# Performance work log

Hardware: AMD Instinct MI355X
Metric: run time of the kernel (lower is better)

Reference implementation:

```python
import jax, jax.numpy as jnp
import numpy as np


def setup_inputs() -> dict:
    key = jax.random.key(0)
    ks = jax.random.split(key, 10)
    B, HD, CD = 8192, 1024, 1024
    stdv = 1.0 / np.sqrt(HD)
    inp = {
        "hprev": jax.random.normal(ks[0], (B, HD), dtype=jnp.float32),
        "cprev": jax.random.normal(ks[1], (B, CD), dtype=jnp.float32),
        "w_hi": jax.random.uniform(ks[2], (HD, CD), jnp.float32, -stdv, stdv),
        "b_hi": jax.random.uniform(ks[3], (1, CD), jnp.float32, -stdv, stdv),
        "w_hf": jax.random.uniform(ks[4], (HD, CD), jnp.float32, -stdv, stdv),
        "b_hf": jax.random.uniform(ks[5], (1, CD), jnp.float32, -stdv, stdv),
        "w_hg": jax.random.uniform(ks[6], (HD, CD), jnp.float32, -stdv, stdv),
        "b_hg": jax.random.uniform(ks[7], (1, CD), jnp.float32, -stdv, stdv),
        "w_ho": jax.random.uniform(ks[8], (HD, CD), jnp.float32, -stdv, stdv),
        "b_ho": jax.random.uniform(ks[9], (1, CD), jnp.float32, -stdv, stdv),
    }
    return inp


def reference(hprev, cprev, w_hi, b_hi, w_hf, b_hf, w_hg, b_hg, w_ho, b_ho):
    # LSTM cell gates driven only by previous hidden state.
    i = jax.nn.sigmoid(hprev @ w_hi + b_hi)   # input gate  [B, CD]
    f = jax.nn.sigmoid(hprev @ w_hf + b_hf)   # forget gate [B, CD]
    g = jnp.tanh(hprev @ w_hg + b_hg)         # cell candidate
    o = jax.nn.sigmoid(hprev @ w_ho + b_ho)   # output gate
    cprime = f * cprev + i * g
    hprime = o * jnp.tanh(cprime)
    return (hprime, cprime)
```

## Files before the change

kernel.cpp:

```cpp
#include <hip/hip_runtime.h>
#include <hip/hip_bf16.h>
#include <stdint.h>

typedef short short8 __attribute__((ext_vector_type(8)));
typedef float f32x4 __attribute__((ext_vector_type(4)));
typedef unsigned short ushort4v __attribute__((ext_vector_type(4)));

#define MDIM 8192
#define KDIM 1024
#define NDIM 1024

#define BM 128
#define BN 64
#define BK 64
#define NKSTEP (KDIM / BK)


__device__ __forceinline__ unsigned short f2bf(float f) {
  union { float f; unsigned int u; } v; v.f = f;
  unsigned int u = v.u;
  u += 0x7fffu + ((u >> 16) & 1u);
  return (unsigned short)(u >> 16);
}

__device__ __forceinline__ void load_lds16(const void* gsrc, void* ldst) {
  __builtin_amdgcn_global_load_lds(
      (__attribute__((address_space(1))) void*)gsrc,
      (__attribute__((address_space(3))) void*)ldst,
      16, 0, 0);
}

__device__ __forceinline__ float fast_sigmoid(float x) {
  return 1.0f / (1.0f + __expf(-x));
}

__device__ __forceinline__ float fast_tanh(float x) {
  x = fminf(30.0f, fmaxf(-30.0f, x));
  float e = __expf(-2.0f * x);
  return (1.0f - e) / (1.0f + e);
}


__global__ void convert_h_kernel(const float* __restrict__ in,
                                 unsigned short* __restrict__ out, int n4) {
  int idx = blockIdx.x * blockDim.x + threadIdx.x;
  int stride = gridDim.x * blockDim.x;
  for (int i = idx; i < n4; i += stride) {
    float4 v = reinterpret_cast<const float4*>(in)[i];
    ushort4v o;
    o.x = f2bf(v.x); o.y = f2bf(v.y); o.z = f2bf(v.z); o.w = f2bf(v.w);
    reinterpret_cast<ushort4v*>(out)[i] = o;
  }
}

__global__ void convert_w_kernel(const float* __restrict__ w0,
                                 const float* __restrict__ w1,
                                 const float* __restrict__ w2,
                                 const float* __restrict__ w3,
                                 unsigned short* __restrict__ wT) {
  __shared__ float tile[64][65];
  int g = blockIdx.z;
  const float* w = (g == 0) ? w0 : (g == 1) ? w1 : (g == 2) ? w2 : w3;
  int k0 = blockIdx.y * 64;
  int n0 = blockIdx.x * 64;
  int tx = threadIdx.x;
  int ty = threadIdx.y;
#pragma unroll
  for (int j = 0; j < 16; ++j) {
    int kk = ty * 16 + j;
    tile[kk][tx] = w[(size_t)(k0 + kk) * NDIM + n0 + tx];
  }
  __syncthreads();
  unsigned short* dst = wT + (size_t)g * NDIM * KDIM;
#pragma unroll
  for (int j = 0; j < 16; ++j) {
    int nn = ty * 16 + j;
    dst[(size_t)(n0 + nn) * KDIM + k0 + tx] = f2bf(tile[tx][nn]);
  }
}


__global__ __launch_bounds__(256, 2) void lstm_fused_gemm(
    const unsigned short* __restrict__ hbf,
    const unsigned short* __restrict__ wT,
    const float* __restrict__ cprev,
    const float* __restrict__ b_i, const float* __restrict__ b_f,
    const float* __restrict__ b_g, const float* __restrict__ b_o,
    float* __restrict__ out)
{
  __shared__ unsigned char lds[48 * 1024];
  const int tid = threadIdx.x;
  const int lane = tid & 63;
  const int wave = tid >> 6;

  int bid = blockIdx.x;
  int swz = (bid & 7) * 128 + (bid >> 3);
  int mb = swz >> 4;
  int nb = swz & 15;
  int brow = mb * BM;
  int bcol = nb * BN;

  const int wr = wave >> 1, wc = wave & 1;
  const int wrow = wr * 64, wcol = wc * 32;

  uint32_t offA[4], offB[8];
#pragma unroll
  for (int j = 0; j < 4; ++j) {
    int c = j * 256 + tid;
    int row = c >> 3, slot = c & 7;
    offA[j] = (uint32_t)((brow + row) * (KDIM * 2) + ((slot ^ (row & 7)) * 16));
  }
#pragma unroll
  for (int j = 0; j < 8; ++j) {
    int c = j * 256 + tid;
    int g = c >> 9;
    int row = (c >> 3) & 63;
    int slot = c & 7;
    offB[j] = (uint32_t)((g * NDIM + bcol + row) * (KDIM * 2) +
                         ((slot ^ (row & 7)) * 16));
  }

  const int h = lane >> 4;
  const int r15 = lane & 15;
  const int s = lane & 7;

  f32x4 acc[4][4][2];
#pragma unroll
  for (int g = 0; g < 4; ++g)
#pragma unroll
    for (int mf = 0; mf < 4; ++mf)
#pragma unroll
      for (int nf = 0; nf < 2; ++nf)
        acc[g][mf][nf] = (f32x4){0.f, 0.f, 0.f, 0.f};

  const char* hbase = (const char*)hbf;
  const char* wbase = (const char*)wT;

  for (int t = 0; t < NKSTEP; ++t) {
    const char* ha = hbase + t * 128;
    const char* wa = wbase + t * 128;
#pragma unroll
    for (int j = 0; j < 4; ++j)
      load_lds16(ha + offA[j], lds + tid * 16 + j * 4096);
#pragma unroll
    for (int j = 0; j < 8; ++j)
      load_lds16(wa + offB[j], lds + 16384 + tid * 16 + j * 4096);
    __syncthreads();

#pragma unroll
    for (int kk = 0; kk < 2; ++kk) {
      short8 a[4];
#pragma unroll
      for (int mf = 0; mf < 4; ++mf) {
        int off = (wrow + mf * 16 + r15) * 128 + (((kk * 4 + h) ^ s) * 16);
        a[mf] = *reinterpret_cast<const short8*>(lds + off);
      }
#pragma unroll
      for (int g = 0; g < 4; ++g) {
#pragma unroll
        for (int nf = 0; nf < 2; ++nf) {
          int off = 16384 + g * 8192 +
                    (wcol + nf * 16 + r15) * 128 + (((kk * 4 + h) ^ s) * 16);
          short8 b = *reinterpret_cast<const short8*>(lds + off);
#pragma unroll
          for (int mf = 0; mf < 4; ++mf)
            acc[g][mf][nf] = __builtin_amdgcn_mfma_f32_16x16x32_bf16(
                a[mf], b, acc[g][mf][nf], 0, 0, 0);
        }
      }
    }
    __syncthreads();
  }

  const size_t outCstride = (size_t)MDIM * NDIM;
#pragma unroll
  for (int nf = 0; nf < 2; ++nf) {
    int cc = bcol + wcol + nf * 16 + r15;
    float bi = b_i[cc];
    float bff = b_f[cc];
    float bg = b_g[cc];
    float bo = b_o[cc];
#pragma unroll
    for (int mf = 0; mf < 4; ++mf) {
#pragma unroll
      for (int j = 0; j < 4; ++j) {
        int rr = brow + wrow + mf * 16 + h * 4 + j;
        size_t base = (size_t)rr * NDIM + cc;
        float pi = acc[0][mf][nf][j] + bi;
        float pf = acc[1][mf][nf][j] + bff;
        float pg = acc[2][mf][nf][j] + bg;
        float po = acc[3][mf][nf][j] + bo;
        float iv = fast_sigmoid(pi);
        float fv = fast_sigmoid(pf);
        float gv = fast_tanh(pg);
        float ov = fast_sigmoid(po);
        float cp = fv * cprev[base] + iv * gv;
        float hp = ov * fast_tanh(cp);
        out[base] = hp;
        out[outCstride + base] = cp;
      }
    }
  }
}


extern "C" void kernel_launch(void* const* d_in, const int* in_sizes, int n_in,
                              void* d_out, int out_size, void* d_ws, size_t ws_size,
                              hipStream_t stream) {
  const float* hprev = (const float*)d_in[0];
  const float* cprev = (const float*)d_in[1];
  const float* w_hi  = (const float*)d_in[2];
  const float* b_hi  = (const float*)d_in[3];
  const float* w_hf  = (const float*)d_in[4];
  const float* b_hf  = (const float*)d_in[5];
  const float* w_hg  = (const float*)d_in[6];
  const float* b_hg  = (const float*)d_in[7];
  const float* w_ho  = (const float*)d_in[8];
  const float* b_ho  = (const float*)d_in[9];
  float* out = (float*)d_out;

  unsigned short* hbf = (unsigned short*)d_ws;
  unsigned short* wT  = (unsigned short*)((char*)d_ws + (size_t)MDIM * KDIM * 2);

  convert_h_kernel<<<2048, 256, 0, stream>>>(hprev, hbf, MDIM * KDIM / 4);
  convert_w_kernel<<<dim3(16, 16, 4), dim3(64, 4, 1), 0, stream>>>(
      w_hi, w_hf, w_hg, w_ho, wT);
  lstm_fused_gemm<<<1024, 256, 0, stream>>>(hbf, wT, cprev,
                                            b_hi, b_hf, b_hg, b_ho, out);
}
```

Baseline: 96.46 us.

## Restructure fused LSTM GEMM into double-buffered 256x64 tiles with interleaved staging

Replaces the single-buffered 128x64 block GEMM with 512-thread blocks computing 256-row tiles. It uses a 128KB double-buffered LDS ring and splits each K-step into halves, so global-to-LDS loads for the next tile are issued between MFMA clusters. Explicit barriers, waitcnt and setprio control the overlap. The aim is to hide global load latency and raise reuse of the weight tiles, at the cost of dropping the LDS XOR swizzle (possible bank conflicts) and limiting occupancy to one large block per CU because of the LDS footprint.

New measurement: 103.1 us. 6.9% more time.

```diff
diff --git a/kernel.cpp b/kernel.cpp
--- a/kernel.cpp
+++ b/kernel.cpp
@@ -9,11 +9,7 @@
 #define MDIM 8192
 #define KDIM 1024
 #define NDIM 1024
-
-#define BM 128
-#define BN 64
-#define BK 64
-#define NKSTEP (KDIM / BK)
+#define NKT  16
 
 
 __device__ __forceinline__ unsigned short f2bf(float f) {
@@ -80,7 +76,31 @@
 }
 
 
-__global__ __launch_bounds__(256, 2) void lstm_fused_gemm(
+#define LDS_BUF   65536
+#define LDS_KH    16384
+#define LDS_B_OFF 32768
+
+#define STAGE_A(kh, h, nb_, tn) \
+  load_lds16(hb + aoff + (h) * 262144 + (tn) * 128 + (kh) * 64, \
+             lds + (nb_) + (kh) * LDS_KH + (h) * 8192 + tid * 16)
+#define STAGE_B(kh, h, nb_, tn) \
+  load_lds16(wb + ((h) ? boff1 : boff0) + (tn) * 128 + (kh) * 64, \
+             lds + (nb_) + LDS_B_OFF + (kh) * LDS_KH + (h) * 8192 + tid * 16)
+
+#define RD_A(cb_, kk, m) \
+  (*(const short8*)(lds + (cb_) + (kk) * LDS_KH + \
+                    (wr * 128 + (m) * 16 + r15) * 64 + hh * 16))
+#define RD_B(cb_, kk, g) \
+  (*(const short8*)(lds + (cb_) + LDS_B_OFF + (kk) * LDS_KH + \
+                    ((g) * 64 + wc * 16 + r15) * 64 + hh * 16))
+
+#define BARRIER() __builtin_amdgcn_s_barrier()
+#define WAIT_LGKM0() do { \
+    asm volatile("s_waitcnt lgkmcnt(0)" ::: "memory"); \
+    __builtin_amdgcn_sched_barrier(0); } while (0)
+#define WAIT_VM4() asm volatile("s_waitcnt vmcnt(4)" ::: "memory")
+
+__global__ __launch_bounds__(512, 2) void lstm_fused_gemm(
     const unsigned short* __restrict__ hbf,
     const unsigned short* __restrict__ wT,
     const float* __restrict__ cprev,
@@ -88,117 +108,179 @@
     const float* __restrict__ b_g, const float* __restrict__ b_o,
     float* __restrict__ out)
 {
-  __shared__ unsigned char lds[48 * 1024];
-  const int tid = threadIdx.x;
+  extern __shared__ unsigned char lds[];
+  const int tid  = threadIdx.x;
   const int lane = tid & 63;
   const int wave = tid >> 6;
+  const int wr = wave >> 2;
+  const int wc = wave & 3;
+  const int r15 = lane & 15;
+  const int hh  = lane >> 4;
 
   int bid = blockIdx.x;
-  int swz = (bid & 7) * 128 + (bid >> 3);
-  int mb = swz >> 4;
-  int nb = swz & 15;
-  int brow = mb * BM;
-  int bcol = nb * BN;
-
-  const int wr = wave >> 1, wc = wave & 1;
-  const int wrow = wr * 64, wcol = wc * 32;
-
-  uint32_t offA[4], offB[8];
-#pragma unroll
-  for (int j = 0; j < 4; ++j) {
-    int c = j * 256 + tid;
-    int row = c >> 3, slot = c & 7;
-    offA[j] = (uint32_t)((brow + row) * (KDIM * 2) + ((slot ^ (row & 7)) * 16));
-  }
-#pragma unroll
-  for (int j = 0; j < 8; ++j) {
-    int c = j * 256 + tid;
-    int g = c >> 9;
-    int row = (c >> 3) & 63;
-    int slot = c & 7;
-    offB[j] = (uint32_t)((g * NDIM + bcol + row) * (KDIM * 2) +
-                         ((slot ^ (row & 7)) * 16));
-  }
-
-  const int h = lane >> 4;
-  const int r15 = lane & 15;
-  const int s = lane & 7;
-
-  f32x4 acc[4][4][2];
+  int loc = bid >> 3;
+  int mb = (bid & 7) * 4 + (loc >> 4);
+  int nb = loc & 15;
+  int brow = mb * 256;
+  int bcol = nb * 64;
+
+  const char* hb = (const char*)hbf;
+  const char* wb = (const char*)wT;
+  const int q  = tid & 3;
+  const int sr = tid >> 2;
+  const uint32_t aoff  = (uint32_t)((brow + sr) * 2048 + q * 16);
+  const uint32_t boff0 = (uint32_t)((((sr >> 6)) * 1024 + bcol + (sr & 63)) * 2048 + q * 16);
+  const uint32_t boff1 = (uint32_t)(((2 + (sr >> 6)) * 1024 + bcol + (sr & 63)) * 2048 + q * 16);
+
+  f32x4 acc[4][8];
 #pragma unroll
   for (int g = 0; g < 4; ++g)
 #pragma unroll
-    for (int mf = 0; mf < 4; ++mf)
-#pragma unroll
-      for (int nf = 0; nf < 2; ++nf)
-        acc[g][mf][nf] = (f32x4){0.f, 0.f, 0.f, 0.f};
-
-  const char* hbase = (const char*)hbf;
-  const char* wbase = (const char*)wT;
-
-  for (int t = 0; t < NKSTEP; ++t) {
-    const char* ha = hbase + t * 128;
-    const char* wa = wbase + t * 128;
-#pragma unroll
-    for (int j = 0; j < 4; ++j)
-      load_lds16(ha + offA[j], lds + tid * 16 + j * 4096);
-#pragma unroll
-    for (int j = 0; j < 8; ++j)
-      load_lds16(wa + offB[j], lds + 16384 + tid * 16 + j * 4096);
-    __syncthreads();
-
-#pragma unroll
-    for (int kk = 0; kk < 2; ++kk) {
-      short8 a[4];
-#pragma unroll
-      for (int mf = 0; mf < 4; ++mf) {
-        int off = (wrow + mf * 16 + r15) * 128 + (((kk * 4 + h) ^ s) * 16);
-        a[mf] = *reinterpret_cast<const short8*>(lds + off);
-      }
-#pragma unroll
-      for (int g = 0; g < 4; ++g) {
-#pragma unroll
-        for (int nf = 0; nf < 2; ++nf) {
-          int off = 16384 + g * 8192 +
-                    (wcol + nf * 16 + r15) * 128 + (((kk * 4 + h) ^ s) * 16);
-          short8 b = *reinterpret_cast<const short8*>(lds + off);
-#pragma unroll
-          for (int mf = 0; mf < 4; ++mf)
-            acc[g][mf][nf] = __builtin_amdgcn_mfma_f32_16x16x32_bf16(
-                a[mf], b, acc[g][mf][nf], 0, 0, 0);
-        }
-      }
-    }
-    __syncthreads();
-  }
-
-  const size_t outCstride = (size_t)MDIM * NDIM;
-#pragma unroll
-  for (int nf = 0; nf < 2; ++nf) {
-    int cc = bcol + wcol + nf * 16 + r15;
-    float bi = b_i[cc];
-    float bff = b_f[cc];
-    float bg = b_g[cc];
-    float bo = b_o[cc];
-#pragma unroll
-    for (int mf = 0; mf < 4; ++mf) {
-#pragma unroll
-      for (int j = 0; j < 4; ++j) {
-        int rr = brow + wrow + mf * 16 + h * 4 + j;
-        size_t base = (size_t)rr * NDIM + cc;
-        float pi = acc[0][mf][nf][j] + bi;
-        float pf = acc[1][mf][nf][j] + bff;
-        float pg = acc[2][mf][nf][j] + bg;
-        float po = acc[3][mf][nf][j] + bo;
-        float iv = fast_sigmoid(pi);
-        float fv = fast_sigmoid(pf);
-        float gv = fast_tanh(pg);
-        float ov = fast_sigmoid(po);
-        float cp = fv * cprev[base] + iv * gv;
-        float hp = ov * fast_tanh(cp);
-        out[base] = hp;
-        out[outCstride + base] = cp;
-      }
+    for (int m = 0; m < 8; ++m)
+      acc[g][m] = (f32x4){0.f, 0.f, 0.f, 0.f};
+
+  uint32_t cb = 0, nbuf = LDS_BUF;
+
+  STAGE_A(0, 0, cb, 0); STAGE_A(0, 1, cb, 0);
+  STAGE_B(0, 0, cb, 0); STAGE_B(0, 1, cb, 0);
+  STAGE_A(1, 0, cb, 0); STAGE_A(1, 1, cb, 0);
+  STAGE_B(1, 0, cb, 0); STAGE_B(1, 1, cb, 0);
+  WAIT_VM4();
+  BARRIER();
+
+  for (int t = 0; t < NKT; ++t) {
+    const int tn = (t + 1) & (NKT - 1);
+
+    short8 B0 = RD_B(cb, 0, 0), B1 = RD_B(cb, 0, 1),
+           B2 = RD_B(cb, 0, 2), B3 = RD_B(cb, 0, 3);
+    short8 A0 = RD_A(cb, 0, 0), A1 = RD_A(cb, 0, 1),
+           A2 = RD_A(cb, 0, 2), A3 = RD_A(cb, 0, 3);
+    STAGE_A(0, 0, nbuf, tn); STAGE_A(0, 1, nbuf, tn);
+    BARRIER();
+    WAIT_LGKM0();
+    __builtin_amdgcn_s_setprio(1);
+    acc[0][0] = __builtin_amdgcn_mfma_f32_16x16x32_bf16(A0, B0, acc[0][0], 0, 0, 0);
+    acc[1][0] = __builtin_amdgcn_mfma_f32_16x16x32_bf16(A0, B1, acc[1][0], 0, 0, 0);
+    acc[2][0] = __builtin_amdgcn_mfma_f32_16x16x32_bf16(A0, B2, acc[2][0], 0, 0, 0);
+    acc[3][0] = __builtin_amdgcn_mfma_f32_16x16x32_bf16(A0, B3, acc[3][0], 0, 0, 0);
+    acc[0][1] = __builtin_amdgcn_mfma_f32_16x16x32_bf16(A1, B0, acc[0][1], 0, 0, 0);
+    acc[1][1] = __builtin_amdgcn_mfma_f32_16x16x32_bf16(A1, B1, acc[1][1], 0, 0, 0);
+    acc[2][1] = __builtin_amdgcn_mfma_f32_16x16x32_bf16(A1, B2, acc[2][1], 0, 0, 0);
+    acc[3][1] = __builtin_amdgcn_mfma_f32_16x16x32_bf16(A1, B3, acc[3][1], 0, 0, 0);
+    acc[0][2] = __builtin_amdgcn_mfma_f32_16x16x32_bf16(A2, B0, acc[0][2], 0, 0, 0);
+    acc[1][2] = __builtin_amdgcn_mfma_f32_16x16x32_bf16(A2, B1, acc[1][2], 0, 0, 0);
+    acc[2][2] = __builtin_amdgcn_mfma_f32_16x16x32_bf16(A2, B2, acc[2][2], 0, 0, 0);
+    acc[3][2] = __builtin_amdgcn_mfma_f32_16x16x32_bf16(A2, B3, acc[3][2], 0, 0, 0);
+    acc[0][3] = __builtin_amdgcn_mfma_f32_16x16x32_bf16(A3, B0, acc[0][3], 0, 0, 0);
+    acc[1][3] = __builtin_amdgcn_mfma_f32_16x16x32_bf16(A3, B1, acc[1][3], 0, 0, 0);
+    acc[2][3] = __builtin_amdgcn_mfma_f32_16x16x32_bf16(A3, B2, acc[2][3], 0, 0, 0);
+    acc[3][3] = __builtin_amdgcn_mfma_f32_16x16x32_bf16(A3, B3, acc[3][3], 0, 0, 0);
+    __builtin_amdgcn_s_setprio(0);
+    BARRIER();
+
+    short8 A4 = RD_A(cb, 0, 4), A5 = RD_A(cb, 0, 5),
+           A6 = RD_A(cb, 0, 6), A7 = RD_A(cb, 0, 7);
+    STAGE_B(0, 0, nbuf, tn); STAGE_B(0, 1, nbuf, tn);
+    BARRIER();
+    WAIT_LGKM0();
+    __builtin_amdgcn_s_setprio(1);
+    acc[0][4] = __builtin_amdgcn_mfma_f32_16x16x32_bf16(A4, B0, acc[0][4], 0, 0, 0);
+    acc[1][4] = __builtin_amdgcn_mfma_f32_16x16x32_bf16(A4, B1, acc[1][4], 0, 0, 0);
+    acc[2][4] = __builtin_amdgcn_mfma_f32_16x16x32_bf16(A4, B2, acc[2][4], 0, 0, 0);
+    acc[3][4] = __builtin_amdgcn_mfma_f32_16x16x32_bf16(A4, B3, acc[3][4], 0, 0, 0);
+    acc[0][5] = __builtin_amdgcn_mfma_f32_16x16x32_bf16(A5, B0, acc[0][5], 0, 0, 0);
+    acc[1][5] = __builtin_amdgcn_mfma_f32_16x16x32_bf16(A5, B1, acc[1][5], 0, 0, 0);
+    acc[2][5] = __builtin_amdgcn_mfma_f32_16x16x32_bf16(A5, B2, acc[2][5], 0, 0, 0);
+    acc[3][5] = __builtin_amdgcn_mfma_f32_16x16x32_bf16(A5, B3, acc[3][5], 0, 0, 0);
+    acc[0][6] = __builtin_amdgcn_mfma_f32_16x16x32_bf16(A6, B0, acc[0][6], 0, 0, 0);
+    acc[1][6] = __builtin_amdgcn_mfma_f32_16x16x32_bf16(A6, B1, acc[1][6], 0, 0, 0);
+    acc[2][6] = __builtin_amdgcn_mfma_f32_16x16x32_bf16(A6, B2, acc[2][6], 0, 0, 0);
+    acc[3][6] = __builtin_amdgcn_mfma_f32_16x16x32_bf16(A6, B3, acc[3][6], 0, 0, 0);
+    acc[0][7] = __builtin_amdgcn_mfma_f32_16x16x32_bf16(A7, B0, acc[0][7], 0, 0, 0);
+    acc[1][7] = __builtin_amdgcn_mfma_f32_16x16x32_bf16(A7, B1, acc[1][7], 0, 0, 0);
+    acc[2][7] = __builtin_amdgcn_mfma_f32_16x16x32_bf16(A7, B2, acc[2][7], 0, 0, 0);
+    acc[3][7] = __builtin_amdgcn_mfma_f32_16x16x32_bf16(A7, B3, acc[3][7], 0, 0, 0);
+    __builtin_amdgcn_s_setprio(0);
+    WAIT_VM4();
+    BARRIER();
+
+    B0 = RD_B(cb, 1, 0); B1 = RD_B(cb, 1, 1);
+    B2 = RD_B(cb, 1, 2); B3 = RD_B(cb, 1, 3);
+    A0 = RD_A(cb, 1, 0); A1 = RD_A(cb, 1, 1);
+    A2 = RD_A(cb, 1, 2); A3 = RD_A(cb, 1, 3);
+    STAGE_A(1, 0, nbuf, tn); STAGE_A(1, 1, nbuf, tn);
+    BARRIER();
+    WAIT_LGKM0();
+    __builtin_amdgcn_s_setprio(1);
+    acc[0][0] = __builtin_amdgcn_mfma_f32_16x16x32_bf16(A0, B0, acc[0][0], 0, 0, 0);
+    acc[1][0] = __builtin_amdgcn_mfma_f32_16x16x32_bf16(A0, B1, acc[1][0], 0, 0, 0);
+    acc[2][0] = __builtin_amdgcn_mfma_f32_16x16x32_bf16(A0, B2, acc[2][0], 0, 0, 0);
+    acc[3][0] = __builtin_amdgcn_mfma_f32_16x16x32_bf16(A0, B3, acc[3][0], 0, 0, 0);
+    acc[0][1] = __builtin_amdgcn_mfma_f32_16x16x32_bf16(A1, B0, acc[0][1], 0, 0, 0);
+    acc[1][1] = __builtin_amdgcn_mfma_f32_16x16x32_bf16(A1, B1, acc[1][1], 0, 0, 0);
+    acc[2][1] = __builtin_amdgcn_mfma_f32_16x16x32_bf16(A1, B2, acc[2][1], 0, 0, 0);
+    acc[3][1] = __builtin_amdgcn_mfma_f32_16x16x32_bf16(A1, B3, acc[3][1], 0, 0, 0);
+    acc[0][2] = __builtin_amdgcn_mfma_f32_16x16x32_bf16(A2, B0, acc[0][2], 0, 0, 0);
+    acc[1][2] = __builtin_amdgcn_mfma_f32_16x16x32_bf16(A2, B1, acc[1][2], 0, 0, 0);
+    acc[2][2] = __builtin_amdgcn_mfma_f32_16x16x32_bf16(A2, B2, acc[2][2], 0, 0, 0);
+    acc[3][2] = __builtin_amdgcn_mfma_f32_16x16x32_bf16(A2, B3, acc[3][2], 0, 0, 0);
+    acc[0][3] = __builtin_amdgcn_mfma_f32_16x16x32_bf16(A3, B0, acc[0][3], 0, 0, 0);
+    acc[1][3] = __builtin_amdgcn_mfma_f32_16x16x32_bf16(A3, B1, acc[1][3], 0, 0, 0);
+    acc[2][3] = __builtin_amdgcn_mfma_f32_16x16x32_bf16(A3, B2, acc[2][3], 0, 0, 0);
+    acc[3][3] = __builtin_amdgcn_mfma_f32_16x16x32_bf16(A3, B3, acc[3][3], 0, 0, 0);
+    __builtin_amdgcn_s_setprio(0);
+    BARRIER();
+
+    A4 = RD_A(cb, 1, 4); A5 = RD_A(cb, 1, 5);
+    A6 = RD_A(cb, 1, 6); A7 = RD_A(cb, 1, 7);
+    STAGE_B(1, 0, nbuf, tn); STAGE_B(1, 1, nbuf, tn);
+    BARRIER();
+    WAIT_LGKM0();
+    __builtin_amdgcn_s_setprio(1);
+    acc[0][4] = __builtin_amdgcn_mfma_f32_16x16x32_bf16(A4, B0, acc[0][4], 0, 0, 0);
+    acc[1][4] = __builtin_amdgcn_mfma_f32_16x16x32_bf16(A4, B1, acc[1][4], 0, 0, 0);
+    acc[2][4] = __builtin_amdgcn_mfma_f32_16x16x32_bf16(A4, B2, acc[2][4], 0, 0, 0);
+    acc[3][4] = __builtin_amdgcn_mfma_f32_16x16x32_bf16(A4, B3, acc[3][4], 0, 0, 0);
+    acc[0][5] = __builtin_amdgcn_mfma_f32_16x16x32_bf16(A5, B0, acc[0][5], 0, 0, 0);
+    acc[1][5] = __builtin_amdgcn_mfma_f32_16x16x32_bf16(A5, B1, acc[1][5], 0, 0, 0);
+    acc[2][5] = __builtin_amdgcn_mfma_f32_16x16x32_bf16(A5, B2, acc[2][5], 0, 0, 0);
+    acc[3][5] = __builtin_amdgcn_mfma_f32_16x16x32_bf16(A5, B3, acc[3][5], 0, 0, 0);
+    acc[0][6] = __builtin_amdgcn_mfma_f32_16x16x32_bf16(A6, B0, acc[0][6], 0, 0, 0);
+    acc[1][6] = __builtin_amdgcn_mfma_f32_16x16x32_bf16(A6, B1, acc[1][6], 0, 0, 0);
+    acc[2][6] = __builtin_amdgcn_mfma_f32_16x16x32_bf16(A6, B2, acc[2][6], 0, 0, 0);
+    acc[3][6] = __builtin_amdgcn_mfma_f32_16x16x32_bf16(A6, B3, acc[3][6], 0, 0, 0);
+    acc[0][7] = __builtin_amdgcn_mfma_f32_16x16x32_bf16(A7, B0, acc[0][7], 0, 0, 0);
+    acc[1][7] = __builtin_amdgcn_mfma_f32_16x16x32_bf16(A7, B1, acc[1][7], 0, 0, 0);
+    acc[2][7] = __builtin_amdgcn_mfma_f32_16x16x32_bf16(A7, B2, acc[2][7], 0, 0, 0);
+    acc[3][7] = __builtin_amdgcn_mfma_f32_16x16x32_bf16(A7, B3, acc[3][7], 0, 0, 0);
+    __builtin_amdgcn_s_setprio(0);
+    WAIT_VM4();
+    BARRIER();
+
+    uint32_t tmp = cb; cb = nbuf; nbuf = tmp;
+  }
+
+  const size_t outC = (size_t)MDIM * NDIM;
+  const int cc = bcol + wc * 16 + r15;
+  const float bi = b_i[cc], bff = b_f[cc], bg = b_g[cc], bo = b_o[cc];
+#pragma unroll
+  for (int m = 0; m < 8; ++m) {
+#pragma unroll
+    for (int j = 0; j < 4; ++j) {
+      int rr = brow + wr * 128 + m * 16 + hh * 4 + j;
+      size_t base = (size_t)rr * NDIM + cc;
+      float pi = acc[0][m][j] + bi;
+      float pf = acc[1][m][j] + bff;
+      float pg = acc[2][m][j] + bg;
+      float po = acc[3][m][j] + bo;
+      float iv = fast_sigmoid(pi);
+      float fv = fast_sigmoid(pf);
+      float gv = fast_tanh(pg);
+      float ov = fast_sigmoid(po);
+      float cp = fv * cprev[base] + iv * gv;
+      float hp = ov * fast_tanh(cp);
+      out[base] = hp;
+      out[outC + base] = cp;
     }
   }
 }
@@ -225,6 +307,6 @@
   convert_h_kernel<<<2048, 256, 0, stream>>>(hprev, hbf, MDIM * KDIM / 4);
   convert_w_kernel<<<dim3(16, 16, 4), dim3(64, 4, 1), 0, stream>>>(
       w_hi, w_hf, w_hg, w_ho, wT);
-  lstm_fused_gemm<<<1024, 256, 0, stream>>>(hbf, wT, cprev,
-                                            b_hi, b_hf, b_hg, b_ho, out);
-}
+  lstm_fused_gemm<<<512, 512, 131072, stream>>>(hbf, wT, cprev,
+                                                b_hi, b_hf, b_hg, b_ho, out);
+}
```

## Rewrite fused LSTM GEMM with 4-stage LDS ring buffer and 512-thread tiles

Applied to the files above, without the earlier changes.

Replaces the single-buffered, sync-per-step GEMM with a 256x64 (per gate) tile computed by 8 waves. It uses a 4-slot LDS ring buffer (128KB dynamic shared memory), prefetching three K-chunks ahead with global_load_lds and interleaving staging with MFMA using explicit s_barrier, waitcnt and setprio. The aim is to hide global-load latency and raise data reuse per block, with a new swizzled LDS layout. The cost is large LDS use, which limits occupancy to about one block per CU, plus fragile hand-written wait counts and barriers.

Measured after the change: 101.2 us. 4.9% more time.

```diff
diff --git a/kernel.cpp b/kernel.cpp
--- a/kernel.cpp
+++ b/kernel.cpp
@@ -9,11 +9,7 @@
 #define MDIM 8192
 #define KDIM 1024
 #define NDIM 1024
-
-#define BM 128
-#define BN 64
-#define BK 64
-#define NKSTEP (KDIM / BK)
+#define NHALF 32
 
 
 __device__ __forceinline__ unsigned short f2bf(float f) {
@@ -80,7 +76,65 @@
 }
 
 
-__global__ __launch_bounds__(256, 2) void lstm_fused_gemm(
+#define SLOT_SZ 32768
+#define S0 0
+#define S1 32768
+#define S2 65536
+#define S3 98304
+
+#define BARRIER() __builtin_amdgcn_s_barrier()
+#define WAIT_LGKM0() do { \
+    asm volatile("s_waitcnt lgkmcnt(0)" ::: "memory"); \
+    __builtin_amdgcn_sched_barrier(0); } while (0)
+#define WAIT_VM8() asm volatile("s_waitcnt vmcnt(8)" ::: "memory")
+
+#define STAGE_A_H(koff, T) do { \
+    load_lds16(hb + srcA0 + (koff), lds + (T) + tid * 16); \
+    load_lds16(hb + srcA1 + (koff), lds + (T) + 8192 + tid * 16); } while (0)
+#define STAGE_B_H(koff, T) do { \
+    load_lds16(wb + srcB0 + (koff), lds + (T) + 16384 + tid * 16); \
+    load_lds16(wb + srcB1 + (koff), lds + (T) + 16384 + 8192 + tid * 16); } while (0)
+
+#define MFMA16(mb_) do { \
+  _Pragma("unroll") \
+  for (int mi = 0; mi < 4; ++mi) { \
+    _Pragma("unroll") \
+    for (int g = 0; g < 4; ++g) \
+      acc[g][(mb_) + mi] = __builtin_amdgcn_mfma_f32_16x16x32_bf16( \
+          Af[mi], Bf[g], acc[g][(mb_) + mi], 0, 0, 0); \
+  } } while (0)
+
+#define HALF(hidx, S, T) do { \
+    const uint32_t ko = (uint32_t)(((hidx) + 3) & (NHALF - 1)) * 64; \
+     \
+    short8 Bf[4], Af[4]; \
+    _Pragma("unroll") \
+    for (int g = 0; g < 4; ++g) \
+      Bf[g] = *(const short8*)(lds + (S) + 16384 + g * 4096 + b_off); \
+    _Pragma("unroll") \
+    for (int mi = 0; mi < 4; ++mi) \
+      Af[mi] = *(const short8*)(lds + (S) + a_off + mi * 1024); \
+    STAGE_A_H(ko, T); \
+    BARRIER(); \
+    WAIT_LGKM0(); \
+    __builtin_amdgcn_s_setprio(1); \
+    MFMA16(0); \
+    __builtin_amdgcn_s_setprio(0); \
+    BARRIER(); \
+     \
+    _Pragma("unroll") \
+    for (int mi = 0; mi < 4; ++mi) \
+      Af[mi] = *(const short8*)(lds + (S) + a_off + (4 + mi) * 1024); \
+    STAGE_B_H(ko, T); \
+    BARRIER(); \
+    WAIT_LGKM0(); \
+    __builtin_amdgcn_s_setprio(1); \
+    MFMA16(4); \
+    __builtin_amdgcn_s_setprio(0); \
+    WAIT_VM8(); \
+    BARRIER(); } while (0)
+
+__global__ __launch_bounds__(512, 2) void lstm_fused_gemm(
     const unsigned short* __restrict__ hbf,
     const unsigned short* __restrict__ wT,
     const float* __restrict__ cprev,
@@ -88,117 +142,81 @@
     const float* __restrict__ b_g, const float* __restrict__ b_o,
     float* __restrict__ out)
 {
-  __shared__ unsigned char lds[48 * 1024];
-  const int tid = threadIdx.x;
+  extern __shared__ unsigned char lds[];
+  const int tid  = threadIdx.x;
   const int lane = tid & 63;
   const int wave = tid >> 6;
+  const int wr = wave >> 2;
+  const int wc = wave & 3;
+  const int r15 = lane & 15;
+  const int hh  = lane >> 4;
 
   int bid = blockIdx.x;
-  int swz = (bid & 7) * 128 + (bid >> 3);
-  int mb = swz >> 4;
-  int nb = swz & 15;
-  int brow = mb * BM;
-  int bcol = nb * BN;
-
-  const int wr = wave >> 1, wc = wave & 1;
-  const int wrow = wr * 64, wcol = wc * 32;
-
-  uint32_t offA[4], offB[8];
-#pragma unroll
-  for (int j = 0; j < 4; ++j) {
-    int c = j * 256 + tid;
-    int row = c >> 3, slot = c & 7;
-    offA[j] = (uint32_t)((brow + row) * (KDIM * 2) + ((slot ^ (row & 7)) * 16));
-  }
-#pragma unroll
-  for (int j = 0; j < 8; ++j) {
-    int c = j * 256 + tid;
-    int g = c >> 9;
-    int row = (c >> 3) & 63;
-    int slot = c & 7;
-    offB[j] = (uint32_t)((g * NDIM + bcol + row) * (KDIM * 2) +
-                         ((slot ^ (row & 7)) * 16));
-  }
-
-  const int h = lane >> 4;
-  const int r15 = lane & 15;
-  const int s = lane & 7;
-
-  f32x4 acc[4][4][2];
+  int loc = bid >> 3;
+  int mb = (bid & 7) * 4 + (loc >> 4);
+  int nb = loc & 15;
+  int brow = mb * 256;
+  int bcol = nb * 64;
+
+  const char* hb = (const char*)hbf;
+  const char* wb = (const char*)wT;
+
+  const int sD = tid & 7;
+  const int pB = tid >> 3;
+  const int u  = sD ^ (pB & 7);
+  const int c16 = (u & 3) * 16;
+  const int rA0 = 2 * pB + (u >> 2);
+  const int rA1 = 128 + rA0;
+  const uint32_t srcA0 = (uint32_t)(brow + rA0) * 2048 + c16;
+  const uint32_t srcA1 = (uint32_t)(brow + rA1) * 2048 + c16;
+  const uint32_t srcB0 = (uint32_t)((rA0 >> 6) * 1024 + bcol + (rA0 & 63)) * 2048 + c16;
+  const uint32_t srcB1 = (uint32_t)((rA1 >> 6) * 1024 + bcol + (rA1 & 63)) * 2048 + c16;
+
+  const int slot16 = (((((r15 & 1) << 2) | hh) ^ (r15 >> 1)) * 16);
+  const uint32_t a_off = (uint32_t)(wr * 64 + (r15 >> 1)) * 128 + slot16;
+  const uint32_t b_off = (uint32_t)(wc * 8 + (r15 >> 1)) * 128 + slot16;
+
+  f32x4 acc[4][8];
 #pragma unroll
   for (int g = 0; g < 4; ++g)
 #pragma unroll
-    for (int mf = 0; mf < 4; ++mf)
-#pragma unroll
-      for (int nf = 0; nf < 2; ++nf)
-        acc[g][mf][nf] = (f32x4){0.f, 0.f, 0.f, 0.f};
-
-  const char* hbase = (const char*)hbf;
-  const char* wbase = (const char*)wT;
-
-  for (int t = 0; t < NKSTEP; ++t) {
-    const char* ha = hbase + t * 128;
-    const char* wa = wbase + t * 128;
-#pragma unroll
-    for (int j = 0; j < 4; ++j)
-      load_lds16(ha + offA[j], lds + tid * 16 + j * 4096);
-#pragma unroll
-    for (int j = 0; j < 8; ++j)
-      load_lds16(wa + offB[j], lds + 16384 + tid * 16 + j * 4096);
-    __syncthreads();
-
-#pragma unroll
-    for (int kk = 0; kk < 2; ++kk) {
-      short8 a[4];
-#pragma unroll
-      for (int mf = 0; mf < 4; ++mf) {
-        int off = (wrow + mf * 16 + r15) * 128 + (((kk * 4 + h) ^ s) * 16);
-        a[mf] = *reinterpret_cast<const short8*>(lds + off);
-      }
-#pragma unroll
-      for (int g = 0; g < 4; ++g) {
-#pragma unroll
-        for (int nf = 0; nf < 2; ++nf) {
-          int off = 16384 + g * 8192 +
-                    (wcol + nf * 16 + r15) * 128 + (((kk * 4 + h) ^ s) * 16);
-          short8 b = *reinterpret_cast<const short8*>(lds + off);
-#pragma unroll
-          for (int mf = 0; mf < 4; ++mf)
-            acc[g][mf][nf] = __builtin_amdgcn_mfma_f32_16x16x32_bf16(
-                a[mf], b, acc[g][mf][nf], 0, 0, 0);
-        }
-      }
-    }
-    __syncthreads();
-  }
-
-  const size_t outCstride = (size_t)MDIM * NDIM;
-#pragma unroll
-  for (int nf = 0; nf < 2; ++nf) {
-    int cc = bcol + wcol + nf * 16 + r15;
-    float bi = b_i[cc];
-    float bff = b_f[cc];
-    float bg = b_g[cc];
-    float bo = b_o[cc];
-#pragma unroll
-    for (int mf = 0; mf < 4; ++mf) {
-#pragma unroll
-      for (int j = 0; j < 4; ++j) {
-        int rr = brow + wrow + mf * 16 + h * 4 + j;
-        size_t base = (size_t)rr * NDIM + cc;
-        float pi = acc[0][mf][nf][j] + bi;
-        float pf = acc[1][mf][nf][j] + bff;
-        float pg = acc[2][mf][nf][j] + bg;
-        float po = acc[3][mf][nf][j] + bo;
-        float iv = fast_sigmoid(pi);
-        float fv = fast_sigmoid(pf);
-        float gv = fast_tanh(pg);
-        float ov = fast_sigmoid(po);
-        float cp = fv * cprev[base] + iv * gv;
-        float hp = ov * fast_tanh(cp);
-        out[base] = hp;
-        out[outCstride + base] = cp;
-      }
+    for (int m = 0; m < 8; ++m)
+      acc[g][m] = (f32x4){0.f, 0.f, 0.f, 0.f};
+
+  STAGE_A_H(0, S0);       STAGE_B_H(0, S0);
+  STAGE_A_H(64, S1);      STAGE_B_H(64, S1);
+  STAGE_A_H(128, S2);     STAGE_B_H(128, S2);
+  WAIT_VM8();
+  BARRIER();
+
+  for (int h = 0; h < NHALF; h += 4) {
+    HALF(h + 0, S0, S3);
+    HALF(h + 1, S1, S0);
+    HALF(h + 2, S2, S1);
+    HALF(h + 3, S3, S2);
+  }
+
+  const size_t outC = (size_t)MDIM * NDIM;
+  const int cc = bcol + wc * 16 + r15;
+  const float bi = b_i[cc], bff = b_f[cc], bg = b_g[cc], bo = b_o[cc];
+#pragma unroll
+  for (int m = 0; m < 8; ++m) {
+#pragma unroll
+    for (int j = 0; j < 4; ++j) {
+      int rr = brow + wr * 128 + m * 16 + hh * 4 + j;
+      size_t base = (size_t)rr * NDIM + cc;
+      float pi = acc[0][m][j] + bi;
+      float pf = acc[1][m][j] + bff;
+      float pg = acc[2][m][j] + bg;
+      float po = acc[3][m][j] + bo;
+      float iv = fast_sigmoid(pi);
+      float fv = fast_sigmoid(pf);
+      float gv = fast_tanh(pg);
+      float ov = fast_sigmoid(po);
+      float cp = fv * cprev[base] + iv * gv;
+      float hp = ov * fast_tanh(cp);
+      out[base] = hp;
+      out[outC + base] = cp;
     }
   }
 }
@@ -225,6 +243,6 @@
   convert_h_kernel<<<2048, 256, 0, stream>>>(hprev, hbf, MDIM * KDIM / 4);
   convert_w_kernel<<<dim3(16, 16, 4), dim3(64, 4, 1), 0, stream>>>(
       w_hi, w_hf, w_hg, w_ho, wT);
-  lstm_fused_gemm<<<1024, 256, 0, stream>>>(hbf, wT, cprev,
-                                            b_hi, b_hf, b_hg, b_ho, out);
-}
+  lstm_fused_gemm<<<512, 512, 131072, stream>>>(hbf, wT, cprev,
+                                                b_hi, b_hf, b_hg, b_ho, out);
+}
```
